# Performance work log

Measured on AMD Instinct MI355X. Metric: run time of the kernel, lower is better.

## Reference

```python
import jax, jax.numpy as jnp
import numpy as np
from jax import lax

INPUT_SIZE = 10
HIDDEN = 128
NUM_CLASSES = 10
B, T = 256, 512


def setup_inputs() -> dict:
    key = jax.random.key(0)
    ks = jax.random.split(key, 12)
    s = 1.0 / np.sqrt(HIDDEN)
    inp = {
        "x": jax.random.normal(ks[0], (B, T, INPUT_SIZE), dtype=jnp.float32),
        # layer 0 (input_size -> hidden), PyTorch gate order [i, f, g, o]
        "w_ih0": jax.random.uniform(ks[1], (4 * HIDDEN, INPUT_SIZE), minval=-s, maxval=s),
        "w_hh0": jax.random.uniform(ks[2], (4 * HIDDEN, HIDDEN), minval=-s, maxval=s),
        "b_ih0": jax.random.uniform(ks[3], (4 * HIDDEN,), minval=-s, maxval=s),
        "b_hh0": jax.random.uniform(ks[4], (4 * HIDDEN,), minval=-s, maxval=s),
        # layer 1 (hidden -> hidden)
        "w_ih1": jax.random.uniform(ks[5], (4 * HIDDEN, HIDDEN), minval=-s, maxval=s),
        "w_hh1": jax.random.uniform(ks[6], (4 * HIDDEN, HIDDEN), minval=-s, maxval=s),
        "b_ih1": jax.random.uniform(ks[7], (4 * HIDDEN,), minval=-s, maxval=s),
        "b_hh1": jax.random.uniform(ks[8], (4 * HIDDEN,), minval=-s, maxval=s),
        # final classifier
        "fc_w": jax.random.uniform(ks[9], (NUM_CLASSES, HIDDEN), minval=-s, maxval=s),
        "fc_b": jax.random.uniform(ks[10], (NUM_CLASSES,), minval=-s, maxval=s),
    }
    return inp


def _lstm_layer(x_seq, w_ih, w_hh, b_ih, b_hh):
    """x_seq: [B, T, D_in] -> hidden sequence [B, T, H]. PyTorch gate order i,f,g,o."""
    b = x_seq.shape[0]
    h_dim = w_hh.shape[1]
    # precompute input contribution as one big GEMM: [B, T, 4H]
    x_gates = jnp.einsum('btd,gd->btg', x_seq, w_ih) + b_ih + b_hh
    x_gates_t = jnp.swapaxes(x_gates, 0, 1)  # [T, B, 4H]

    def step(carry, xg):
        h, c = carry
        gates = xg + h @ w_hh.T  # [B, 4H]
        i, f, g, o = jnp.split(gates, 4, axis=-1)
        i = jax.nn.sigmoid(i)
        f = jax.nn.sigmoid(f)
        g = jnp.tanh(g)
        o = jax.nn.sigmoid(o)
        c_new = f * c + i * g
        h_new = o * jnp.tanh(c_new)
        return (h_new, c_new), h_new

    h0 = jnp.zeros((b, h_dim), dtype=x_seq.dtype)
    c0 = jnp.zeros((b, h_dim), dtype=x_seq.dtype)
    _, hs = lax.scan(step, (h0, c0), x_gates_t)  # hs: [T, B, H]
    return jnp.swapaxes(hs, 0, 1)  # [B, T, H]


def reference(x, w_ih0, w_hh0, b_ih0, b_hh0, w_ih1, w_hh1, b_ih1, b_hh1, fc_w, fc_b):
    h1 = _lstm_layer(x, w_ih0, w_hh0, b_ih0, b_hh0)      # [B, T, H]
    h2 = _lstm_layer(h1, w_ih1, w_hh1, b_ih1, b_hh1)     # [B, T, H]
    last = h2[:, -1, :]                                   # [B, H]
    return last @ fc_w.T + fc_b                           # [B, num_classes]
```

## Files before the change

### kernel.cpp

```cpp
#include <hip/hip_runtime.h>

#define HID   128
#define GATES 512
#define BATCH 256
#define SEQ   512
#define INSZ  10
#define MB    16
#define NBLK  (BATCH / MB)
#define NTHR  512
#define HSTR  136
#define XSTR  40
#define XCH   8
#define HCH   4
#define PCH   8

typedef _Float16 half8  __attribute__((ext_vector_type(8)));
typedef _Float16 half2v __attribute__((ext_vector_type(2)));
typedef float    floatx4 __attribute__((ext_vector_type(4)));

#define MFMA16(A, B, C) __builtin_amdgcn_mfma_f32_16x16x32_f16(A, B, C, 0, 0, 0)

#define KSIG  (-1.4426950408889634f)
#define KTAN  (-2.8853900817779268f)

__device__ __forceinline__ float sigm_pre(float a)
{
    return __builtin_amdgcn_rcpf(1.0f + __builtin_amdgcn_exp2f(a));
}
__device__ __forceinline__ float tanh_pre(float a)
{
    return __builtin_fmaf(2.0f, __builtin_amdgcn_rcpf(1.0f + __builtin_amdgcn_exp2f(a)), -1.0f);
}
__device__ __forceinline__ float tanh_plain(float c)
{
    return tanh_pre(c * KTAN);
}

__device__ __forceinline__ half8 load_wfrag(const float* rowbase, int k0, float scale)
{
    const float4* p = (const float4*)(rowbase + k0);
    float4 a = p[0], b = p[1];
    half8 r;
    r[0] = (_Float16)(a.x * scale); r[1] = (_Float16)(a.y * scale);
    r[2] = (_Float16)(a.z * scale); r[3] = (_Float16)(a.w * scale);
    r[4] = (_Float16)(b.x * scale); r[5] = (_Float16)(b.y * scale);
    r[6] = (_Float16)(b.z * scale); r[7] = (_Float16)(b.w * scale);
    return r;
}

#define XBUF_HALFS (XCH * MB * XSTR)
#define H1C_BUF_HALFS (HCH * MB * HSTR)
#define H0_OFF  20480
#define H2_OFF  34816
#define LDS_BYTES 43520

__device__ __forceinline__ int wait_flag(int* flagp, int needed, int lastf)
{
    if (lastf >= needed) return lastf;
    int f = __hip_atomic_load(flagp, __ATOMIC_RELAXED, __HIP_MEMORY_SCOPE_AGENT);
    while (f < needed) {
        __builtin_amdgcn_s_sleep(2);
        f = __hip_atomic_load(flagp, __ATOMIC_RELAXED, __HIP_MEMORY_SCOPE_AGENT);
    }
    (void)__hip_atomic_load(flagp, __ATOMIC_ACQUIRE, __HIP_MEMORY_SCOPE_AGENT);
    return f;
}

__global__ __launch_bounds__(NTHR, 2)
void lstm_fused(const float* __restrict__ x,
                const float* __restrict__ w_ih0, const float* __restrict__ w_hh0,
                const float* __restrict__ b_ih0, const float* __restrict__ b_hh0,
                const float* __restrict__ w_ih1, const float* __restrict__ w_hh1,
                const float* __restrict__ b_ih1, const float* __restrict__ b_hh1,
                const float* __restrict__ fc_w,  const float* __restrict__ fc_b,
                float* __restrict__ out, _Float16* __restrict__ h1w_all)
{
    const int tid  = threadIdx.x;
    const int lane = tid & 63;
    const int wv   = tid >> 6;
    const int m16  = lane & 15;
    const int quad = lane >> 4;
    const int col  = (wv << 4) + m16;

    const bool producer = (blockIdx.x < NBLK);
    const int  pb = producer ? blockIdx.x : blockIdx.x - NBLK;
    const int  b0 = pb * MB;

    __shared__ __align__(16) char lds[LDS_BYTES];
    _Float16* xs  = (_Float16*)lds;
    _Float16* h0s = (_Float16*)(lds + H0_OFF);
    _Float16* h1c = (_Float16*)lds;
    _Float16* h2s = (_Float16*)(lds + H2_OFF);
    float*    h2f = (float*)lds;

    _Float16* h1w = h1w_all + (size_t)pb * SEQ * MB * HID;
    int* flagp = (int*)out + pb * (MB * 10);

    const float gsc[4] = {KSIG, KSIG, KTAN, KSIG};

    if (producer) {
        half8 Whh0f[4][4];
        half8 Wih0f[4];
        float bias0[4];
#pragma unroll
        for (int g = 0; g < 4; ++g) {
            const int gr = g * HID + col;
            const float sc = gsc[g];
            bias0[g] = (b_ih0[gr] + b_hh0[gr]) * sc;
#pragma unroll
            for (int ks = 0; ks < 4; ++ks)
                Whh0f[g][ks] = load_wfrag(w_hh0 + (size_t)gr * HID, ks * 32 + quad * 8, sc);
            half8 r;
#pragma unroll
            for (int j = 0; j < 8; ++j) {
                int k = quad * 8 + j;
                r[j] = (k < INSZ) ? (_Float16)(w_ih0[gr * INSZ + k] * sc) : (_Float16)0.0f;
            }
            Wih0f[g] = r;
        }

        for (int i = tid; i < (H0_OFF + 8704) / 4; i += NTHR) ((int*)lds)[i] = 0;

        if (tid < 128) {
            const int s = tid >> 4, m = tid & 15;
            const float2* xp = (const float2*)(x + ((size_t)(b0 + m) * SEQ + s) * INSZ);
            _Float16* dst = xs + (s * MB + m) * XSTR;
#pragma unroll
            for (int p = 0; p < 5; ++p) {
                float2 v = xp[p];
                half2v h; h[0] = (_Float16)v.x; h[1] = (_Float16)v.y;
                *(half2v*)(dst + 2 * p) = h;
            }
        }
        __syncthreads();

        float c0[4] = {0.f, 0.f, 0.f, 0.f};
        float2 xr[5];
        for (int t = 0; t < SEQ; ++t) {
            const int rb = t & 1, wb = rb ^ 1;
            const int sub = t & 7;
            if (sub == 0 && t + XCH < SEQ && tid < 128) {
                const int s = tid >> 4, m = tid & 15;
                const float2* xp = (const float2*)(x + ((size_t)(b0 + m) * SEQ + (t + XCH + s)) * INSZ);
#pragma unroll
                for (int p = 0; p < 5; ++p) xr[p] = xp[p];
            }
            const _Float16* hb = h0s + rb * (MB * HSTR) + m16 * HSTR + quad * 8;
            half8 ha0 = *(const half8*)(hb);
            half8 ha1 = *(const half8*)(hb + 32);
            half8 ha2 = *(const half8*)(hb + 64);
            half8 ha3 = *(const half8*)(hb + 96);
            half8 xa  = *(const half8*)(xs + ((t >> 3) & 1) * XBUF_HALFS + (sub * MB + m16) * XSTR + quad * 8);

            floatx4 a0 = {bias0[0], bias0[0], bias0[0], bias0[0]};
            floatx4 a1 = {bias0[1], bias0[1], bias0[1], bias0[1]};
            floatx4 a2 = {bias0[2], bias0[2], bias0[2], bias0[2]};
            floatx4 a3 = {bias0[3], bias0[3], bias0[3], bias0[3]};
            a0 = MFMA16(xa, Wih0f[0], a0); a1 = MFMA16(xa, Wih0f[1], a1);
            a2 = MFMA16(xa, Wih0f[2], a2); a3 = MFMA16(xa, Wih0f[3], a3);
            a0 = MFMA16(ha0, Whh0f[0][0], a0); a1 = MFMA16(ha0, Whh0f[1][0], a1);
            a2 = MFMA16(ha0, Whh0f[2][0], a2); a3 = MFMA16(ha0, Whh0f[3][0], a3);
            a0 = MFMA16(ha1, Whh0f[0][1], a0); a1 = MFMA16(ha1, Whh0f[1][1], a1);
            a2 = MFMA16(ha1, Whh0f[2][1], a2); a3 = MFMA16(ha1, Whh0f[3][1], a3);
            a0 = MFMA16(ha2, Whh0f[0][2], a0); a1 = MFMA16(ha2, Whh0f[1][2], a1);
            a2 = MFMA16(ha2, Whh0f[2][2], a2); a3 = MFMA16(ha2, Whh0f[3][2], a3);
            a0 = MFMA16(ha3, Whh0f[0][3], a0); a1 = MFMA16(ha3, Whh0f[1][3], a1);
            a2 = MFMA16(ha3, Whh0f[2][3], a2); a3 = MFMA16(ha3, Whh0f[3][3], a3);

            if (sub == 2 && t + 6 < SEQ && tid < 128) {
                const int s = tid >> 4, m = tid & 15;
                _Float16* dst = xs + (((t >> 3) + 1) & 1) * XBUF_HALFS + (s * MB + m) * XSTR;
#pragma unroll
                for (int p = 0; p < 5; ++p) {
                    half2v h; h[0] = (_Float16)xr[p].x; h[1] = (_Float16)xr[p].y;
                    *(half2v*)(dst + 2 * p) = h;
                }
            }
            _Float16* hw = h0s + wb * (MB * HSTR);
#pragma unroll
            for (int e = 0; e < 4; ++e) {
                float iv = sigm_pre(a0[e]);
                float fv = sigm_pre(a1[e]);
                float gv = tanh_pre(a2[e]);
                float ov = sigm_pre(a3[e]);
                c0[e] = __builtin_fmaf(fv, c0[e], iv * gv);
                float hv = ov * tanh_plain(c0[e]);
                _Float16 hh = (_Float16)hv;
                const int row = quad * 4 + e;
                hw[row * HSTR + col] = hh;
                h1w[((size_t)t * MB + row) * HID + col] = hh;
            }
            __syncthreads();
            if ((t & (PCH - 1)) == (PCH - 1) && tid == 0) {
                __threadfence();
                __hip_atomic_store(flagp, t + 1, __ATOMIC_RELEASE, __HIP_MEMORY_SCOPE_AGENT);
            }
        }
        return;
    }

    half8 Wih1f[4][4], Whh1f[4][4];
    float bias1[4];
#pragma unroll
    for (int g = 0; g < 4; ++g) {
        const int gr = g * HID + col;
        const float sc = gsc[g];
        bias1[g] = (b_ih1[gr] + b_hh1[gr]) * sc;
#pragma unroll
        for (int ks = 0; ks < 4; ++ks) {
            Wih1f[g][ks] = load_wfrag(w_ih1 + (size_t)gr * HID, ks * 32 + quad * 8, sc);
            Whh1f[g][ks] = load_wfrag(w_hh1 + (size_t)gr * HID, ks * 32 + quad * 8, sc);
        }
    }
    for (int i = tid; i < 2176; i += NTHR) ((int*)(lds + H2_OFF))[i] = 0;

    int lastf = 0;
    lastf = wait_flag(flagp, PCH, lastf);

#pragma unroll
    for (int r = 0; r < 2; ++r) {
        const int fi = tid + NTHR * r;
        const int ef = fi * 8;
        const int s = ef >> 11, rem = ef & 2047;
        const int m = rem >> 7, k0 = rem & 127;
        int4 v = *(const int4*)(h1w + ef);
        *(int4*)(h1c + (s * MB + m) * HSTR + k0) = v;
    }
    __syncthreads();

    float c1[4] = {0.f, 0.f, 0.f, 0.f};
    int4 hr0, hr1;
    for (int t = 0; t < SEQ; ++t) {
        const int rb = t & 1, wb = rb ^ 1;
        const int sub = t & 3;
        const int hc = t >> 2;
        if (sub == 0 && t + HCH < SEQ) {
            lastf = wait_flag(flagp, t + 2 * HCH, lastf);
            const _Float16* src = h1w + (size_t)(hc + 1) * (HCH * MB * HID);
            hr0 = *(const int4*)(src + tid * 8);
            hr1 = *(const int4*)(src + (tid + NTHR) * 8);
        }
        const _Float16* h1b = h1c + (hc & 1) * H1C_BUF_HALFS + (sub * MB + m16) * HSTR + quad * 8;
        half8 p0 = *(const half8*)(h1b);
        half8 p1 = *(const half8*)(h1b + 32);
        half8 p2 = *(const half8*)(h1b + 64);
        half8 p3 = *(const half8*)(h1b + 96);
        const _Float16* h2b = h2s + rb * (MB * HSTR) + m16 * HSTR + quad * 8;
        half8 q0 = *(const half8*)(h2b);
        half8 q1 = *(const half8*)(h2b + 32);
        half8 q2 = *(const half8*)(h2b + 64);
        half8 q3 = *(const half8*)(h2b + 96);

        floatx4 a0 = {bias1[0], bias1[0], bias1[0], bias1[0]};
        floatx4 a1 = {bias1[1], bias1[1], bias1[1], bias1[1]};
        floatx4 a2 = {bias1[2], bias1[2], bias1[2], bias1[2]};
        floatx4 a3 = {bias1[3], bias1[3], bias1[3], bias1[3]};
        a0 = MFMA16(p0, Wih1f[0][0], a0); a1 = MFMA16(p0, Wih1f[1][0], a1);
        a2 = MFMA16(p0, Wih1f[2][0], a2); a3 = MFMA16(p0, Wih1f[3][0], a3);
        a0 = MFMA16(p1, Wih1f[0][1], a0); a1 = MFMA16(p1, Wih1f[1][1], a1);
        a2 = MFMA16(p1, Wih1f[2][1], a2); a3 = MFMA16(p1, Wih1f[3][1], a3);
        a0 = MFMA16(p2, Wih1f[0][2], a0); a1 = MFMA16(p2, Wih1f[1][2], a1);
        a2 = MFMA16(p2, Wih1f[2][2], a2); a3 = MFMA16(p2, Wih1f[3][2], a3);
        a0 = MFMA16(p3, Wih1f[0][3], a0); a1 = MFMA16(p3, Wih1f[1][3], a1);
        a2 = MFMA16(p3, Wih1f[2][3], a2); a3 = MFMA16(p3, Wih1f[3][3], a3);
        a0 = MFMA16(q0, Whh1f[0][0], a0); a1 = MFMA16(q0, Whh1f[1][0], a1);
        a2 = MFMA16(q0, Whh1f[2][0], a2); a3 = MFMA16(q0, Whh1f[3][0], a3);
        a0 = MFMA16(q1, Whh1f[0][1], a0); a1 = MFMA16(q1, Whh1f[1][1], a1);
        a2 = MFMA16(q1, Whh1f[2][1], a2); a3 = MFMA16(q1, Whh1f[3][1], a3);
        a0 = MFMA16(q2, Whh1f[0][2], a0); a1 = MFMA16(q2, Whh1f[1][2], a1);
        a2 = MFMA16(q2, Whh1f[2][2], a2); a3 = MFMA16(q2, Whh1f[3][2], a3);
        a0 = MFMA16(q3, Whh1f[0][3], a0); a1 = MFMA16(q3, Whh1f[1][3], a1);
        a2 = MFMA16(q3, Whh1f[2][3], a2); a3 = MFMA16(q3, Whh1f[3][3], a3);

        if (sub == 2 && t + 2 < SEQ) {
            _Float16* dstb = h1c + ((hc + 1) & 1) * H1C_BUF_HALFS;
            {
                int ef = tid * 8;
                int s = ef >> 11, rem = ef & 2047, m = rem >> 7, k0 = rem & 127;
                *(int4*)(dstb + (s * MB + m) * HSTR + k0) = hr0;
                ef = (tid + NTHR) * 8;
                s = ef >> 11; rem = ef & 2047; m = rem >> 7; k0 = rem & 127;
                *(int4*)(dstb + (s * MB + m) * HSTR + k0) = hr1;
            }
        }
        _Float16* hw2 = h2s + wb * (MB * HSTR);
#pragma unroll
        for (int e = 0; e < 4; ++e) {
            float iv = sigm_pre(a0[e]);
            float fv = sigm_pre(a1[e]);
            float gv = tanh_pre(a2[e]);
            float ov = sigm_pre(a3[e]);
            c1[e] = __builtin_fmaf(fv, c1[e], iv * gv);
            float hv = ov * tanh_plain(c1[e]);
            const int row = quad * 4 + e;
            hw2[row * HSTR + col] = (_Float16)hv;
            if (t == SEQ - 1) h2f[row * 132 + col] = hv;
        }
        __syncthreads();
    }

    if (tid < 160) {
        const int cls = tid >> 4, b = tid & 15;
        float a = fc_b[cls];
        const float* wr = fc_w + cls * HID;
#pragma unroll 8
        for (int k = 0; k < HID; ++k) a += wr[k] * h2f[b * 132 + k];
        out[(size_t)(b0 + b) * 10 + cls] = a;
    }
}

extern "C" void kernel_launch(void* const* d_in, const int* in_sizes, int n_in,
                              void* d_out, int out_size, void* d_ws, size_t ws_size,
                              hipStream_t stream) {
    (void)in_sizes; (void)n_in; (void)out_size; (void)ws_size;
    const float* x     = (const float*)d_in[0];
    const float* w_ih0 = (const float*)d_in[1];
    const float* w_hh0 = (const float*)d_in[2];
    const float* b_ih0 = (const float*)d_in[3];
    const float* b_hh0 = (const float*)d_in[4];
    const float* w_ih1 = (const float*)d_in[5];
    const float* w_hh1 = (const float*)d_in[6];
    const float* b_ih1 = (const float*)d_in[7];
    const float* b_hh1 = (const float*)d_in[8];
    const float* fc_w  = (const float*)d_in[9];
    const float* fc_b  = (const float*)d_in[10];
    float* out = (float*)d_out;
    _Float16* h1w = (_Float16*)d_ws;

    hipMemsetAsync(d_out, 0, BATCH * 10 * sizeof(float), stream);
    lstm_fused<<<2 * NBLK, NTHR, 0, stream>>>(x, w_ih0, w_hh0, b_ih0, b_hh0,
                                              w_ih1, w_hh1, b_ih1, b_hh1,
                                              fc_w, fc_b, out, h1w);
}
```

Before: 670.4 us.

## Stage layer-0 hidden states in an 8-slot LDS ring and flush in coalesced bursts

The layer-0 producer now writes each step's hidden state into an 8-deep LDS history ring instead of double buffering, and no longer issues scattered 2-byte global stores every step. Every 8 steps the block copies the ring to global memory with 16-byte vector stores, waits for vmcnt, then publishes the flag. Per-step __syncthreads is replaced with an lgkmcnt-only wait plus s_barrier so the barrier does not drain outstanding global memory ops. This raises LDS use per block and concentrates global traffic into bursts on the producer's critical path.

```diff
diff --git a/kernel.cpp b/kernel.cpp
--- a/kernel.cpp
+++ b/kernel.cpp
@@ -20,6 +20,10 @@
 
 #define MFMA16(A, B, C) __builtin_amdgcn_mfma_f32_16x16x32_f16(A, B, C, 0, 0, 0)
 
+#define LGKM_BARRIER() do { \
+    asm volatile("s_waitcnt lgkmcnt(0)" ::: "memory"); \
+    __builtin_amdgcn_s_barrier(); } while (0)
+
 #define KSIG  (-1.4426950408889634f)
 #define KTAN  (-2.8853900817779268f)
 
@@ -50,9 +54,9 @@
 
 #define XBUF_HALFS (XCH * MB * XSTR)
 #define H1C_BUF_HALFS (HCH * MB * HSTR)
-#define H0_OFF  20480
-#define H2_OFF  34816
-#define LDS_BYTES 43520
+#define HIST_OFF 20480
+#define H2_OFF   34816
+#define LDS_BYTES 55296
 
 __device__ __forceinline__ int wait_flag(int* flagp, int needed, int lastf)
 {
@@ -87,11 +91,11 @@
     const int  b0 = pb * MB;
 
     __shared__ __align__(16) char lds[LDS_BYTES];
-    _Float16* xs  = (_Float16*)lds;
-    _Float16* h0s = (_Float16*)(lds + H0_OFF);
-    _Float16* h1c = (_Float16*)lds;
-    _Float16* h2s = (_Float16*)(lds + H2_OFF);
-    float*    h2f = (float*)lds;
+    _Float16* xs   = (_Float16*)lds;
+    _Float16* hist = (_Float16*)(lds + HIST_OFF);
+    _Float16* h1c  = (_Float16*)lds;
+    _Float16* h2s  = (_Float16*)(lds + H2_OFF);
+    float*    h2f  = (float*)lds;
 
     _Float16* h1w = h1w_all + (size_t)pb * SEQ * MB * HID;
     int* flagp = (int*)out + pb * (MB * 10);
@@ -119,7 +123,7 @@
             Wih0f[g] = r;
         }
 
-        for (int i = tid; i < (H0_OFF + 8704) / 4; i += NTHR) ((int*)lds)[i] = 0;
+        for (int i = tid; i < LDS_BYTES / 4; i += NTHR) ((int*)lds)[i] = 0;
 
         if (tid < 128) {
             const int s = tid >> 4, m = tid & 15;
@@ -137,7 +141,6 @@
         float c0[4] = {0.f, 0.f, 0.f, 0.f};
         float2 xr[5];
         for (int t = 0; t < SEQ; ++t) {
-            const int rb = t & 1, wb = rb ^ 1;
             const int sub = t & 7;
             if (sub == 0 && t + XCH < SEQ && tid < 128) {
                 const int s = tid >> 4, m = tid & 15;
@@ -145,7 +148,7 @@
 #pragma unroll
                 for (int p = 0; p < 5; ++p) xr[p] = xp[p];
             }
-            const _Float16* hb = h0s + rb * (MB * HSTR) + m16 * HSTR + quad * 8;
+            const _Float16* hb = hist + ((t + 7) & 7) * (MB * HSTR) + m16 * HSTR + quad * 8;
             half8 ha0 = *(const half8*)(hb);
             half8 ha1 = *(const half8*)(hb + 32);
             half8 ha2 = *(const half8*)(hb + 64);
@@ -176,7 +179,7 @@
                     *(half2v*)(dst + 2 * p) = h;
                 }
             }
-            _Float16* hw = h0s + wb * (MB * HSTR);
+            _Float16* hw = hist + (t & 7) * (MB * HSTR);
 #pragma unroll
             for (int e = 0; e < 4; ++e) {
                 float iv = sigm_pre(a0[e]);
@@ -185,15 +188,28 @@
                 float ov = sigm_pre(a3[e]);
                 c0[e] = __builtin_fmaf(fv, c0[e], iv * gv);
                 float hv = ov * tanh_plain(c0[e]);
-                _Float16 hh = (_Float16)hv;
                 const int row = quad * 4 + e;
-                hw[row * HSTR + col] = hh;
-                h1w[((size_t)t * MB + row) * HID + col] = hh;
-            }
-            __syncthreads();
-            if ((t & (PCH - 1)) == (PCH - 1) && tid == 0) {
-                __threadfence();
-                __hip_atomic_store(flagp, t + 1, __ATOMIC_RELEASE, __HIP_MEMORY_SCOPE_AGENT);
+                hw[row * HSTR + col] = (_Float16)hv;
+            }
+            if (sub == 7) {
+                LGKM_BARRIER();
+#pragma unroll
+                for (int r = 0; r < 4; ++r) {
+                    const int e = tid + NTHR * r;
+                    const int c16 = e & 15;
+                    const int m   = (e >> 4) & 15;
+                    const int j   = e >> 8;
+                    int4 v = *(const int4*)(hist + (j * MB + m) * HSTR + c16 * 8);
+                    *(int4*)(h1w + ((size_t)(t - 7 + j) * MB + m) * HID + c16 * 8) = v;
+                }
+                asm volatile("s_waitcnt vmcnt(0)" ::: "memory");
+                __builtin_amdgcn_s_barrier();
+                if (tid == 0) {
+                    __threadfence();
+                    __hip_atomic_store(flagp, t + 1, __ATOMIC_RELEASE, __HIP_MEMORY_SCOPE_AGENT);
+                }
+            } else {
+                LGKM_BARRIER();
             }
         }
         return;
@@ -296,7 +312,7 @@
             hw2[row * HSTR + col] = (_Float16)hv;
             if (t == SEQ - 1) h2f[row * 132 + col] = hv;
         }
-        __syncthreads();
+        LGKM_BARRIER();
     }
 
     if (tid < 160) {
```

After: 678.1 us. Within noise of the previous version (+1.1%).

## Batch input-projection MFMAs across four timesteps off the recurrent chain

Applied to the files above, without the earlier changes.

Both LSTM layers now compute the input-to-hidden gate contributions (plus bias) for four timesteps at once, in a burst placed every four steps. Each per-step recurrent update then only runs the four dependent hidden-to-hidden MFMAs per gate, starting from the precomputed accumulator. This shortens the per-step dependent MFMA chain, most noticeably in layer 1, where it drops from eight to four. In exchange, sixteen extra floatx4 accumulators stay live in registers, and the burst still sits before the barrier, so it adds periodic work to the serial path.

```diff
diff --git a/kernel.cpp b/kernel.cpp
--- a/kernel.cpp
+++ b/kernel.cpp
@@ -122,9 +122,9 @@
         for (int i = tid; i < (H0_OFF + 8704) / 4; i += NTHR) ((int*)lds)[i] = 0;
 
         if (tid < 128) {
-            const int s = tid >> 4, m = tid & 15;
-            const float2* xp = (const float2*)(x + ((size_t)(b0 + m) * SEQ + s) * INSZ);
-            _Float16* dst = xs + (s * MB + m) * XSTR;
+            const int sr = tid >> 4, mr = tid & 15;
+            const float2* xp = (const float2*)(x + ((size_t)(b0 + mr) * SEQ + sr) * INSZ);
+            _Float16* dst = xs + (sr * MB + mr) * XSTR;
 #pragma unroll
             for (int p = 0; p < 5; ++p) {
                 float2 v = xp[p];
@@ -136,64 +136,77 @@
 
         float c0[4] = {0.f, 0.f, 0.f, 0.f};
         float2 xr[5];
-        for (int t = 0; t < SEQ; ++t) {
-            const int rb = t & 1, wb = rb ^ 1;
-            const int sub = t & 7;
-            if (sub == 0 && t + XCH < SEQ && tid < 128) {
-                const int s = tid >> 4, m = tid & 15;
-                const float2* xp = (const float2*)(x + ((size_t)(b0 + m) * SEQ + (t + XCH + s)) * INSZ);
-#pragma unroll
-                for (int p = 0; p < 5; ++p) xr[p] = xp[p];
-            }
-            const _Float16* hb = h0s + rb * (MB * HSTR) + m16 * HSTR + quad * 8;
-            half8 ha0 = *(const half8*)(hb);
-            half8 ha1 = *(const half8*)(hb + 32);
-            half8 ha2 = *(const half8*)(hb + 64);
-            half8 ha3 = *(const half8*)(hb + 96);
-            half8 xa  = *(const half8*)(xs + ((t >> 3) & 1) * XBUF_HALFS + (sub * MB + m16) * XSTR + quad * 8);
-
-            floatx4 a0 = {bias0[0], bias0[0], bias0[0], bias0[0]};
-            floatx4 a1 = {bias0[1], bias0[1], bias0[1], bias0[1]};
-            floatx4 a2 = {bias0[2], bias0[2], bias0[2], bias0[2]};
-            floatx4 a3 = {bias0[3], bias0[3], bias0[3], bias0[3]};
-            a0 = MFMA16(xa, Wih0f[0], a0); a1 = MFMA16(xa, Wih0f[1], a1);
-            a2 = MFMA16(xa, Wih0f[2], a2); a3 = MFMA16(xa, Wih0f[3], a3);
-            a0 = MFMA16(ha0, Whh0f[0][0], a0); a1 = MFMA16(ha0, Whh0f[1][0], a1);
-            a2 = MFMA16(ha0, Whh0f[2][0], a2); a3 = MFMA16(ha0, Whh0f[3][0], a3);
-            a0 = MFMA16(ha1, Whh0f[0][1], a0); a1 = MFMA16(ha1, Whh0f[1][1], a1);
-            a2 = MFMA16(ha1, Whh0f[2][1], a2); a3 = MFMA16(ha1, Whh0f[3][1], a3);
-            a0 = MFMA16(ha2, Whh0f[0][2], a0); a1 = MFMA16(ha2, Whh0f[1][2], a1);
-            a2 = MFMA16(ha2, Whh0f[2][2], a2); a3 = MFMA16(ha2, Whh0f[3][2], a3);
-            a0 = MFMA16(ha3, Whh0f[0][3], a0); a1 = MFMA16(ha3, Whh0f[1][3], a1);
-            a2 = MFMA16(ha3, Whh0f[2][3], a2); a3 = MFMA16(ha3, Whh0f[3][3], a3);
-
-            if (sub == 2 && t + 6 < SEQ && tid < 128) {
-                const int s = tid >> 4, m = tid & 15;
-                _Float16* dst = xs + (((t >> 3) + 1) & 1) * XBUF_HALFS + (s * MB + m) * XSTR;
-#pragma unroll
-                for (int p = 0; p < 5; ++p) {
-                    half2v h; h[0] = (_Float16)xr[p].x; h[1] = (_Float16)xr[p].y;
-                    *(half2v*)(dst + 2 * p) = h;
-                }
-            }
-            _Float16* hw = h0s + wb * (MB * HSTR);
-#pragma unroll
-            for (int e = 0; e < 4; ++e) {
-                float iv = sigm_pre(a0[e]);
-                float fv = sigm_pre(a1[e]);
-                float gv = tanh_pre(a2[e]);
-                float ov = sigm_pre(a3[e]);
-                c0[e] = __builtin_fmaf(fv, c0[e], iv * gv);
-                float hv = ov * tanh_plain(c0[e]);
-                _Float16 hh = (_Float16)hv;
-                const int row = quad * 4 + e;
-                hw[row * HSTR + col] = hh;
-                h1w[((size_t)t * MB + row) * HID + col] = hh;
-            }
-            __syncthreads();
-            if ((t & (PCH - 1)) == (PCH - 1) && tid == 0) {
-                __threadfence();
-                __hip_atomic_store(flagp, t + 1, __ATOMIC_RELEASE, __HIP_MEMORY_SCOPE_AGENT);
+        floatx4 xg[4][4];
+
+        auto xburst = [&](int base) {
+            const _Float16* xb = xs + ((base >> 3) & 1) * XBUF_HALFS;
+#pragma unroll
+            for (int k = 0; k < 4; ++k) {
+                half8 xa = *(const half8*)(xb + (((base & 7) + k) * MB + m16) * XSTR + quad * 8);
+#pragma unroll
+                for (int g = 0; g < 4; ++g) {
+                    floatx4 a = {bias0[g], bias0[g], bias0[g], bias0[g]};
+                    a = MFMA16(xa, Wih0f[g], a);
+                    xg[k][g] = a;
+                }
+            }
+        };
+        xburst(0);
+
+        for (int tc = 0; tc < SEQ; tc += 8) {
+#pragma unroll
+            for (int s8 = 0; s8 < 8; ++s8) {
+                const int t = tc + s8;
+                const int sl = s8 & 3;
+                if (s8 == 0 && t + XCH < SEQ && tid < 128) {
+                    const int sr = tid >> 4, mr = tid & 15;
+                    const float2* xp = (const float2*)(x + ((size_t)(b0 + mr) * SEQ + (t + XCH + sr)) * INSZ);
+#pragma unroll
+                    for (int p = 0; p < 5; ++p) xr[p] = xp[p];
+                }
+                const _Float16* hb = h0s + (s8 & 1) * (MB * HSTR) + m16 * HSTR + quad * 8;
+                half8 ha0 = *(const half8*)(hb);
+                half8 ha1 = *(const half8*)(hb + 32);
+                half8 ha2 = *(const half8*)(hb + 64);
+                half8 ha3 = *(const half8*)(hb + 96);
+#pragma unroll
+                for (int g = 0; g < 4; ++g) {
+                    floatx4 a = xg[sl][g];
+                    a = MFMA16(ha0, Whh0f[g][0], a);
+                    a = MFMA16(ha1, Whh0f[g][1], a);
+                    a = MFMA16(ha2, Whh0f[g][2], a);
+                    a = MFMA16(ha3, Whh0f[g][3], a);
+                    xg[sl][g] = a;
+                }
+                if (s8 == 2 && t + 6 < SEQ && tid < 128) {
+                    const int sr = tid >> 4, mr = tid & 15;
+                    _Float16* dst = xs + (((t >> 3) + 1) & 1) * XBUF_HALFS + (sr * MB + mr) * XSTR;
+#pragma unroll
+                    for (int p = 0; p < 5; ++p) {
+                        half2v h; h[0] = (_Float16)xr[p].x; h[1] = (_Float16)xr[p].y;
+                        *(half2v*)(dst + 2 * p) = h;
+                    }
+                }
+                _Float16* hw = h0s + ((s8 & 1) ^ 1) * (MB * HSTR);
+#pragma unroll
+                for (int e = 0; e < 4; ++e) {
+                    float iv = sigm_pre(xg[sl][0][e]);
+                    float fv = sigm_pre(xg[sl][1][e]);
+                    float gv = tanh_pre(xg[sl][2][e]);
+                    float ov = sigm_pre(xg[sl][3][e]);
+                    c0[e] = __builtin_fmaf(fv, c0[e], iv * gv);
+                    float hv = ov * tanh_plain(c0[e]);
+                    _Float16 hh = (_Float16)hv;
+                    const int row = quad * 4 + e;
+                    hw[row * HSTR + col] = hh;
+                    h1w[((size_t)t * MB + row) * HID + col] = hh;
+                }
+                if ((s8 == 3 || s8 == 7) && t + 4 < SEQ) xburst(t + 1);
+                __syncthreads();
+                if (s8 == 7 && tid == 0) {
+                    __threadfence();
+                    __hip_atomic_store(flagp, t + 1, __ATOMIC_RELEASE, __HIP_MEMORY_SCOPE_AGENT);
+                }
             }
         }
         return;
@@ -221,82 +234,88 @@
     for (int r = 0; r < 2; ++r) {
         const int fi = tid + NTHR * r;
         const int ef = fi * 8;
-        const int s = ef >> 11, rem = ef & 2047;
-        const int m = rem >> 7, k0 = rem & 127;
+        const int ss = ef >> 11, rem = ef & 2047;
+        const int mm = rem >> 7, k0 = rem & 127;
         int4 v = *(const int4*)(h1w + ef);
-        *(int4*)(h1c + (s * MB + m) * HSTR + k0) = v;
+        *(int4*)(h1c + (ss * MB + mm) * HSTR + k0) = v;
     }
     __syncthreads();
+
+    floatx4 pg[4][4];
+
+    auto pburst = [&](int base) {
+        const _Float16* sb = h1c + ((base >> 2) & 1) * H1C_BUF_HALFS;
+#pragma unroll
+        for (int k = 0; k < 4; ++k) {
+            const _Float16* pp = sb + (k * MB + m16) * HSTR + quad * 8;
+            half8 f0 = *(const half8*)(pp);
+            half8 f1 = *(const half8*)(pp + 32);
+            half8 f2 = *(const half8*)(pp + 64);
+            half8 f3 = *(const half8*)(pp + 96);
+#pragma unroll
+            for (int g = 0; g < 4; ++g) {
+                floatx4 a = {bias1[g], bias1[g], bias1[g], bias1[g]};
+                a = MFMA16(f0, Wih1f[g][0], a);
+                a = MFMA16(f1, Wih1f[g][1], a);
+                a = MFMA16(f2, Wih1f[g][2], a);
+                a = MFMA16(f3, Wih1f[g][3], a);
+                pg[k][g] = a;
+            }
+        }
+    };
+    pburst(0);
 
     float c1[4] = {0.f, 0.f, 0.f, 0.f};
     int4 hr0, hr1;
-    for (int t = 0; t < SEQ; ++t) {
-        const int rb = t & 1, wb = rb ^ 1;
-        const int sub = t & 3;
-        const int hc = t >> 2;
-        if (sub == 0 && t + HCH < SEQ) {
-            lastf = wait_flag(flagp, t + 2 * HCH, lastf);
-            const _Float16* src = h1w + (size_t)(hc + 1) * (HCH * MB * HID);
-            hr0 = *(const int4*)(src + tid * 8);
-            hr1 = *(const int4*)(src + (tid + NTHR) * 8);
-        }
-        const _Float16* h1b = h1c + (hc & 1) * H1C_BUF_HALFS + (sub * MB + m16) * HSTR + quad * 8;
-        half8 p0 = *(const half8*)(h1b);
-        half8 p1 = *(const half8*)(h1b + 32);
-        half8 p2 = *(const half8*)(h1b + 64);
-        half8 p3 = *(const half8*)(h1b + 96);
-        const _Float16* h2b = h2s + rb * (MB * HSTR) + m16 * HSTR + quad * 8;
-        half8 q0 = *(const half8*)(h2b);
-        half8 q1 = *(const half8*)(h2b + 32);
-        half8 q2 = *(const half8*)(h2b + 64);
-        half8 q3 = *(const half8*)(h2b + 96);
-
-        floatx4 a0 = {bias1[0], bias1[0], bias1[0], bias1[0]};
-        floatx4 a1 = {bias1[1], bias1[1], bias1[1], bias1[1]};
-        floatx4 a2 = {bias1[2], bias1[2], bias1[2], bias1[2]};
-        floatx4 a3 = {bias1[3], bias1[3], bias1[3], bias1[3]};
-        a0 = MFMA16(p0, Wih1f[0][0], a0); a1 = MFMA16(p0, Wih1f[1][0], a1);
-        a2 = MFMA16(p0, Wih1f[2][0], a2); a3 = MFMA16(p0, Wih1f[3][0], a3);
-        a0 = MFMA16(p1, Wih1f[0][1], a0); a1 = MFMA16(p1, Wih1f[1][1], a1);
-        a2 = MFMA16(p1, Wih1f[2][1], a2); a3 = MFMA16(p1, Wih1f[3][1], a3);
-        a0 = MFMA16(p2, Wih1f[0][2], a0); a1 = MFMA16(p2, Wih1f[1][2], a1);
-        a2 = MFMA16(p2, Wih1f[2][2], a2); a3 = MFMA16(p2, Wih1f[3][2], a3);
-        a0 = MFMA16(p3, Wih1f[0][3], a0); a1 = MFMA16(p3, Wih1f[1][3], a1);
-        a2 = MFMA16(p3, Wih1f[2][3], a2); a3 = MFMA16(p3, Wih1f[3][3], a3);
-        a0 = MFMA16(q0, Whh1f[0][0], a0); a1 = MFMA16(q0, Whh1f[1][0], a1);
-        a2 = MFMA16(q0, Whh1f[2][0], a2); a3 = MFMA16(q0, Whh1f[3][0], a3);
-        a0 = MFMA16(q1, Whh1f[0][1], a0); a1 = MFMA16(q1, Whh1f[1][1], a1);
-        a2 = MFMA16(q1, Whh1f[2][1], a2); a3 = MFMA16(q1, Whh1f[3][1], a3);
-        a0 = MFMA16(q2, Whh1f[0][2], a0); a1 = MFMA16(q2, Whh1f[1][2], a1);
-        a2 = MFMA16(q2, Whh1f[2][2], a2); a3 = MFMA16(q2, Whh1f[3][2], a3);
-        a0 = MFMA16(q3, Whh1f[0][3], a0); a1 = MFMA16(q3, Whh1f[1][3], a1);
-        a2 = MFMA16(q3, Whh1f[2][3], a2); a3 = MFMA16(q3, Whh1f[3][3], a3);
-
-        if (sub == 2 && t + 2 < SEQ) {
-            _Float16* dstb = h1c + ((hc + 1) & 1) * H1C_BUF_HALFS;
-            {
+    for (int tc = 0; tc < SEQ; tc += 4) {
+#pragma unroll
+        for (int s = 0; s < 4; ++s) {
+            const int t = tc + s;
+            if (s == 0 && t + HCH < SEQ) {
+                lastf = wait_flag(flagp, t + 2 * HCH, lastf);
+                const _Float16* src = h1w + (size_t)((t >> 2) + 1) * (HCH * MB * HID);
+                hr0 = *(const int4*)(src + tid * 8);
+                hr1 = *(const int4*)(src + (tid + NTHR) * 8);
+            }
+            const _Float16* h2b = h2s + (s & 1) * (MB * HSTR) + m16 * HSTR + quad * 8;
+            half8 q0 = *(const half8*)(h2b);
+            half8 q1 = *(const half8*)(h2b + 32);
+            half8 q2 = *(const half8*)(h2b + 64);
+            half8 q3 = *(const half8*)(h2b + 96);
+#pragma unroll
+            for (int g = 0; g < 4; ++g) {
+                floatx4 a = pg[s][g];
+                a = MFMA16(q0, Whh1f[g][0], a);
+                a = MFMA16(q1, Whh1f[g][1], a);
+                a = MFMA16(q2, Whh1f[g][2], a);
+                a = MFMA16(q3, Whh1f[g][3], a);
+                pg[s][g] = a;
+            }
+            if (s == 2 && t + 2 < SEQ) {
+                _Float16* dstb = h1c + (((t >> 2) + 1) & 1) * H1C_BUF_HALFS;
                 int ef = tid * 8;
-                int s = ef >> 11, rem = ef & 2047, m = rem >> 7, k0 = rem & 127;
-                *(int4*)(dstb + (s * MB + m) * HSTR + k0) = hr0;
+                int ss = ef >> 11, rem = ef & 2047, mm = rem >> 7, k0 = rem & 127;
+                *(int4*)(dstb + (ss * MB + mm) * HSTR + k0) = hr0;
                 ef = (tid + NTHR) * 8;
-                s = ef >> 11; rem = ef & 2047; m = rem >> 7; k0 = rem & 127;
-                *(int4*)(dstb + (s * MB + m) * HSTR + k0) = hr1;
-            }
-        }
-        _Float16* hw2 = h2s + wb * (MB * HSTR);
-#pragma unroll
-        for (int e = 0; e < 4; ++e) {
-            float iv = sigm_pre(a0[e]);
-            float fv = sigm_pre(a1[e]);
-            float gv = tanh_pre(a2[e]);
-            float ov = sigm_pre(a3[e]);
-            c1[e] = __builtin_fmaf(fv, c1[e], iv * gv);
-            float hv = ov * tanh_plain(c1[e]);
-            const int row = quad * 4 + e;
-            hw2[row * HSTR + col] = (_Float16)hv;
-            if (t == SEQ - 1) h2f[row * 132 + col] = hv;
-        }
-        __syncthreads();
+                ss = ef >> 11; rem = ef & 2047; mm = rem >> 7; k0 = rem & 127;
+                *(int4*)(dstb + (ss * MB + mm) * HSTR + k0) = hr1;
+            }
+            _Float16* hw2 = h2s + ((s & 1) ^ 1) * (MB * HSTR);
+#pragma unroll
+            for (int e = 0; e < 4; ++e) {
+                float iv = sigm_pre(pg[s][0][e]);
+                float fv = sigm_pre(pg[s][1][e]);
+                float gv = tanh_pre(pg[s][2][e]);
+                float ov = sigm_pre(pg[s][3][e]);
+                c1[e] = __builtin_fmaf(fv, c1[e], iv * gv);
+                float hv = ov * tanh_plain(c1[e]);
+                const int row = quad * 4 + e;
+                hw2[row * HSTR + col] = (_Float16)hv;
+                if (t == SEQ - 1) h2f[row * 132 + col] = hv;
+            }
+            if (s == 3 && t + 1 < SEQ) pburst(t + 1);
+            __syncthreads();
+        }
     }
 
     if (tid < 160) {
```

Result: faster. 606.7 us (-9.5%).
